# Performance work log

Hardware: AMD Instinct MI355X
Metric: run time of the kernel (lower is better)

The kernel has to match this reference:

```python
import jax, jax.numpy as jnp
import numpy as np

N, L = 131072, 4          # traffic lights, lanes per TL
E, H = 64, 128            # embed_dim, hidden_dim
NH, HD = 4, 16            # num_heads, head_dim (E = NH*HD)
NR, R = 4, 8              # num_regions, region_embed_dim
INIT_LOG_STD = -0.5


def _lin(k, fan_in, shape):
    b = 1.0 / np.sqrt(fan_in)
    return jax.random.uniform(k, shape, minval=-b, maxval=b, dtype=jnp.float32)


def setup_inputs() -> dict:
    key = jax.random.key(0)
    ks = jax.random.split(key, 32)
    inp = {
        "queue": jax.random.uniform(ks[0], (N, L), dtype=jnp.float32),
        "waiting": jax.random.uniform(ks[1], (N, L), dtype=jnp.float32),
        "phase_onehot": jax.random.uniform(ks[2], (N, 4), dtype=jnp.float32),
        "elapsed": jax.random.uniform(ks[3], (N,), dtype=jnp.float32),
        "region_ids": jax.random.randint(ks[4], (N,), 0, NR, dtype=jnp.int32),
        "noise": jax.random.normal(ks[5], (N,), dtype=jnp.float32),
        # lane_mlp: Linear(3,H) -> ReLU -> Linear(H,E) -> ReLU
        "lane_w1": _lin(ks[6], 3, (3, H)), "lane_b1": _lin(ks[7], 3, (H,)),
        "lane_w2": _lin(ks[8], H, (H, E)), "lane_b2": _lin(ks[9], H, (E,)),
        # MultiheadAttention in/out projections
        "attn_in_w": _lin(ks[10], E, (E, 3 * E)), "attn_in_b": jnp.zeros((3 * E,), jnp.float32),
        "attn_out_w": _lin(ks[11], E, (E, E)), "attn_out_b": jnp.zeros((E,), jnp.float32),
        # phase_mlp: Linear(5,H) -> ReLU -> Linear(H,H) -> ReLU
        "phase_w1": _lin(ks[12], 5, (5, H)), "phase_b1": _lin(ks[13], 5, (H,)),
        "phase_w2": _lin(ks[14], H, (H, H)), "phase_b2": _lin(ks[15], H, (H,)),
        # region embedding table
        "region_table": jax.random.normal(ks[16], (NR, R), dtype=jnp.float32),
        # mlp_head: Linear(E+H+R, H) -> ReLU -> Linear(H, 1)
        "head_w1": _lin(ks[17], E + H + R, (E + H + R, H)), "head_b1": _lin(ks[18], E + H + R, (H,)),
        "head_w2": _lin(ks[19], H, (H, 1)), "head_b2": _lin(ks[20], H, (1,)),
        "log_std": jnp.full((1,), INIT_LOG_STD, dtype=jnp.float32),
    }
    return inp


def reference(queue, waiting, phase_onehot, elapsed, region_ids, noise,
              lane_w1, lane_b1, lane_w2, lane_b2,
              attn_in_w, attn_in_b, attn_out_w, attn_out_b,
              phase_w1, phase_b1, phase_w2, phase_b2,
              region_table, head_w1, head_b1, head_w2, head_b2, log_std):
    # --- lane context: tiny MLP + self-attention over L lanes, batched over N TLs ---
    lane_feats = jnp.stack([queue, waiting, jnp.broadcast_to(elapsed[:, None], (N, L))], axis=-1)  # [N,L,3]
    h = jax.nn.relu(lane_feats @ lane_w1 + lane_b1)          # [N,L,H]
    emb = jax.nn.relu(h @ lane_w2 + lane_b2)                 # [N,L,E]

    qkv = emb @ attn_in_w + attn_in_b                        # [N,L,3E]
    q, k, v = jnp.split(qkv, 3, axis=-1)
    def heads(x):  # [N,L,E] -> [N,NH,L,HD]
        return x.reshape(N, L, NH, HD).transpose(0, 2, 1, 3)
    q, k, v = heads(q), heads(k), heads(v)
    scores = jnp.einsum('bhqd,bhkd->bhqk', q, k) / np.sqrt(HD)   # [N,NH,L,L]
    attn = jax.nn.softmax(scores, axis=-1)
    o = jnp.einsum('bhqk,bhkd->bhqd', attn, v)               # [N,NH,L,HD]
    o = o.transpose(0, 2, 1, 3).reshape(N, L, E)
    attn_out = o @ attn_out_w + attn_out_b                   # [N,L,E]
    ctx = attn_out.mean(axis=1)                              # [N,E]

    # --- phase MLP ---
    phase_elapsed = jnp.concatenate([phase_onehot, elapsed[:, None]], axis=-1)  # [N,5]
    ph = jax.nn.relu(phase_elapsed @ phase_w1 + phase_b1)
    phase_emb = jax.nn.relu(ph @ phase_w2 + phase_b2)        # [N,H]

    # --- region embedding (clamped index) ---
    rid = jnp.clip(region_ids, 0, NR - 1)
    region_emb = region_table[rid]                           # [N,R]

    # --- Gaussian head ---
    feat = jnp.concatenate([ctx, phase_emb, region_emb], axis=-1)  # [N,E+H+R]
    means = (jax.nn.relu(feat @ head_w1 + head_b1) @ head_w2 + head_b2)[:, 0]  # [N]

    ls = jnp.broadcast_to(log_std, means.shape)
    std = jnp.exp(ls)
    actions = means + std * noise
    actions_clamped = jnp.clip(actions, -1.0, 1.0)
    log_prob = -0.5 * ((actions - means) ** 2 / (std * std) + 2.0 * ls + np.log(2.0 * np.pi))
    return actions_clamped, log_prob
```

## Files before the change

### kernel.cpp

```cpp
#include <hip/hip_runtime.h>
#include <math.h>

#define N_TL 131072
#define GRID 2048
#define BLK 256

#define NFRAG 70
#define WS_CONST_OFF (NFRAG * 256)
#define NCONST 1346

typedef __attribute__((ext_vector_type(8))) short bfrag;
typedef __attribute__((ext_vector_type(4))) float f32x4;
typedef __attribute__((ext_vector_type(16))) float f32x16;

__device__ __forceinline__ unsigned short f2bf_rne(float x) {
  unsigned int u = __float_as_uint(x);
  return (unsigned short)((u + 0x7fffu + ((u >> 16) & 1u)) >> 16);
}
__device__ __forceinline__ unsigned int pack2(float a, float b) {
  return __builtin_amdgcn_perm(__float_as_uint(b) + 0x8000u,
                               __float_as_uint(a) + 0x8000u, 0x07060302u);
}
__device__ __forceinline__ float lo16(unsigned int u) { return __uint_as_float(u << 16); }
__device__ __forceinline__ float hi16(unsigned int u) { return __uint_as_float(u & 0xffff0000u); }
__device__ __forceinline__ f32x4 mfma16(bfrag a, bfrag b, f32x4 c) {
  return __builtin_amdgcn_mfma_f32_16x16x32_bf16(a, b, c, 0, 0, 0);
}
__device__ __forceinline__ f32x16 mfma32(bfrag a, bfrag b, f32x16 c) {
  return __builtin_amdgcn_mfma_f32_32x32x16_bf16(a, b, c, 0, 0, 0);
}

__device__ __forceinline__ bfrag load_wfragT(const float* __restrict__ w, int ncols,
                                             int col0, int k0, int lane, int K, float scale) {
  const int mm = lane & 15, qq = lane >> 4;
  bfrag f;
  #pragma unroll
  for (int j = 0; j < 8; ++j) {
    const int k = k0 + qq * 8 + j;
    const float v = (k < K) ? w[(size_t)k * ncols + col0 + mm] * scale : 0.f;
    f[j] = (short)f2bf_rne(v);
  }
  return f;
}
__device__ __forceinline__ bfrag load_wfragT32(const float* __restrict__ w, int ncols,
                                               int m0, int k0, int lane, int K, float scale) {
  const int mm = lane & 31, q1 = lane >> 5;
  bfrag f;
  #pragma unroll
  for (int j = 0; j < 8; ++j) {
    const int k = k0 + q1 * 8 + j;
    const float v = (k < K) ? w[(size_t)k * ncols + m0 + mm] * scale : 0.f;
    f[j] = (short)f2bf_rne(v);
  }
  return f;
}

__device__ __forceinline__ bfrag ldfrag(const uint4* __restrict__ WF, int f, int tid) {
  uint4 u = WF[f * 256 + tid];
  return *reinterpret_cast<bfrag*>(&u);
}

__device__ __forceinline__ bfrag ldb32f(const unsigned short* arr, int stride, int row,
                                        int kk, int q1) {
  return *reinterpret_cast<const bfrag*>(&arr[row * stride + kk * 16 + q1 * 8]);
}
__device__ __forceinline__ f32x16 binit32(const float* bias, int chBase, int q1) {
  f32x16 a;
  #pragma unroll
  for (int g = 0; g < 4; ++g) {
    const f32x4 bb = *reinterpret_cast<const f32x4*>(&bias[chBase + g * 8 + q1 * 4]);
    a[g * 4 + 0] = bb[0]; a[g * 4 + 1] = bb[1];
    a[g * 4 + 2] = bb[2]; a[g * 4 + 3] = bb[3];
  }
  return a;
}
__device__ __forceinline__ void st32(unsigned short* arr, int stride, int row,
                                     int chBase, int q1, f32x16 acc, bool relu) {
  #pragma unroll
  for (int g = 0; g < 4; ++g) {
    float a0 = acc[g * 4 + 0], a1 = acc[g * 4 + 1];
    float a2 = acc[g * 4 + 2], a3 = acc[g * 4 + 3];
    if (relu) {
      a0 = fmaxf(a0, 0.f); a1 = fmaxf(a1, 0.f);
      a2 = fmaxf(a2, 0.f); a3 = fmaxf(a3, 0.f);
    }
    uint2 u;
    u.x = pack2(a0, a1);
    u.y = pack2(a2, a3);
    *reinterpret_cast<uint2*>(&arr[row * stride + chBase + g * 8 + q1 * 4]) = u;
  }
}

#define LDBACT(arr, stride, nt, kk) \
  (*reinterpret_cast<const bfrag*>(&(arr)[((nt) * 16 + m) * (stride) + (kk) * 32 + quad * 8]))

__global__ __launch_bounds__(BLK)
void prep_weights(const float* __restrict__ lane_w1, const float* __restrict__ lane_b1,
                  const float* __restrict__ lane_w2, const float* __restrict__ lane_b2,
                  const float* __restrict__ attn_in_w, const float* __restrict__ attn_in_b,
                  const float* __restrict__ attn_out_w, const float* __restrict__ attn_out_b,
                  const float* __restrict__ phase_w1, const float* __restrict__ phase_b1,
                  const float* __restrict__ phase_w2, const float* __restrict__ phase_b2,
                  const float* __restrict__ region_table,
                  const float* __restrict__ head_w1, const float* __restrict__ head_b1,
                  const float* __restrict__ head_w2, const float* __restrict__ head_b2,
                  const float* __restrict__ log_std,
                  uint4* __restrict__ ws) {
  const int f = blockIdx.x;
  const int tid = threadIdx.x;
  const int wv = tid >> 6, lane = tid & 63;
  const int mb = wv >> 1;
  bfrag r;
  if (f < 8) {
    r = load_wfragT32(lane_w2, 64, mb * 32, f * 16, lane, 128, 1.f);
  } else if (f < 20) {
    const int t = (f - 8) >> 2, kk = (f - 8) & 3;
    r = load_wfragT32(attn_in_w, 192, (mb + 2 * t) * 32, kk * 16, lane, 64,
                      t == 0 ? 0.25f : 1.f);
  } else if (f < 22) {
    r = load_wfragT(attn_out_w, 64, wv * 16, (f - 20) * 32, lane, 64, 0.25f);
  } else if (f < 26) {
    const int t = (f - 22) >> 1, kk = (f - 22) & 1;
    r = load_wfragT32(lane_w1, 128, (mb + 2 * t) * 32, kk * 16, lane, 3, 1.f);
  } else if (f < 30) {
    const int t = (f - 26) >> 1, kk = (f - 26) & 1;
    r = load_wfragT32(phase_w1, 128, (mb + 2 * t) * 32, kk * 16, lane, 5, 1.f);
  } else if (f < 46) {
    const int t = (f - 30) >> 3, kk = (f - 30) & 7;
    r = load_wfragT32(phase_w2, 128, (mb + 2 * t) * 32, kk * 16, lane, 128, 1.f);
  } else {
    const int t = (f - 46) / 12, kk = (f - 46) % 12;
    r = load_wfragT32(head_w1, 128, (mb + 2 * t) * 32, kk * 16, lane, 192, 1.f);
  }
  ws[f * 256 + tid] = *reinterpret_cast<uint4*>(&r);

  if (f == 0) {
    float* wc = reinterpret_cast<float*>(ws + WS_CONST_OFF);
    for (int i = tid; i < NCONST; i += BLK) {
      float v;
      if (i < 128)       v = lane_b1[i];
      else if (i < 192)  v = lane_b2[i - 128];
      else if (i < 384)  { const int j = i - 192; v = attn_in_b[j] * ((j < 64) ? 0.25f : 1.f); }
      else if (i < 448)  v = attn_out_b[i - 384];
      else if (i < 576)  v = phase_b1[i - 448];
      else if (i < 704)  v = phase_b2[i - 576];
      else if (i < 1216) {
        const int g = (i - 704) >> 7, c = (i - 704) & 127;
        float a = head_b1[c];
        #pragma unroll
        for (int j = 0; j < 8; ++j) a += region_table[g * 8 + j] * head_w1[(192 + j) * 128 + c];
        v = a;
      }
      else if (i < 1344) v = head_w2[i - 1216];
      else if (i == 1344) v = head_b2[0];
      else               v = log_std[0];
      wc[i] = v;
    }
  }
}

struct alignas(16) SmemF {
  union {
    unsigned short qkv[64 * 200];
    unsigned short h[64 * 136];
    unsigned short ph[64 * 136];
  };
  unsigned short emb[64 * 72];
  unsigned short xbuf[64 * 40];
  unsigned short feat[64 * 200];
  float b1[128], b2[64], bin[192], bout[64];
  float pb1[128], pb2[128];
  float rbias[4][128];
  float hw2[128];
  float consts[2];
  int ridx[64];
};

__global__ __launch_bounds__(BLK, 2)
void fused_policy(const float* __restrict__ queue,
                  const float* __restrict__ waiting,
                  const float* __restrict__ phase_onehot,
                  const float* __restrict__ elapsed,
                  const int* __restrict__ region_ids,
                  const float* __restrict__ noise,
                  const uint4* __restrict__ WF,
                  float* __restrict__ out) {
  __shared__ SmemF S;
  const int tid  = threadIdx.x;
  const int wv   = tid >> 6;
  const int lane = tid & 63;
  const int m    = lane & 15;
  const int quad = lane >> 4;
  const int n32  = lane & 31;
  const int q1   = lane >> 5;
  const int mb   = wv >> 1;
  const int row64 = (wv & 1) * 32 + n32;
  const int n0   = blockIdx.x * 64;

  bfrag wL1[2][2], wL2[8], wQKV[3][4], wOUT2[2];
  #pragma unroll
  for (int kk = 0; kk < 8; ++kk) wL2[kk] = ldfrag(WF, kk, tid);
  #pragma unroll
  for (int t = 0; t < 3; ++t)
    #pragma unroll
    for (int kk = 0; kk < 4; ++kk) wQKV[t][kk] = ldfrag(WF, 8 + t * 4 + kk, tid);
  #pragma unroll
  for (int kk = 0; kk < 2; ++kk) wOUT2[kk] = ldfrag(WF, 20 + kk, tid);
  #pragma unroll
  for (int t = 0; t < 2; ++t)
    #pragma unroll
    for (int kk = 0; kk < 2; ++kk) wL1[t][kk] = ldfrag(WF, 22 + t * 2 + kk, tid);

  {
    const float2* src = reinterpret_cast<const float2*>(WF + WS_CONST_OFF);
    float2* dst = reinterpret_cast<float2*>(&S.b1[0]);
    for (int i = tid; i < NCONST / 2; i += BLK) dst[i] = src[i];
  }
  if (tid < 64) {
    int r = region_ids[n0 + tid];
    S.ridx[tid] = r < 0 ? 0 : (r > 3 ? 3 : r);
  }
  {
    const int r = tid >> 2, seg = tid & 3;
    uint4 z = {0, 0, 0, 0};
    if (seg == 0) {
      const int gl = n0 * 4 + r;
      z.x = pack2(queue[gl], waiting[gl]);
      z.y = pack2(elapsed[n0 + (r >> 2)], 0.f);
    }
    *reinterpret_cast<uint4*>(&S.xbuf[r * 40 + seg * 8]) = z;
  }
  __syncthreads();

  #pragma unroll 1
  for (int s = 0; s < 4; ++s) {
    const int tl0 = n0 + s * 16;

    {
      f32x16 acc[2];
      #pragma unroll
      for (int t = 0; t < 2; ++t) acc[t] = binit32(S.b1, (mb + 2 * t) * 32, q1);
      #pragma unroll
      for (int kk = 0; kk < 2; ++kk) {
        const bfrag b = ldb32f(S.xbuf, 40, row64, kk, q1);
        acc[0] = mfma32(wL1[0][kk], b, acc[0]);
        acc[1] = mfma32(wL1[1][kk], b, acc[1]);
      }
      #pragma unroll
      for (int t = 0; t < 2; ++t) st32(S.h, 136, row64, (mb + 2 * t) * 32, q1, acc[t], true);
    }
    __syncthreads();

    {
      f32x16 acc = binit32(S.b2, mb * 32, q1);
      #pragma unroll
      for (int kk = 0; kk < 8; ++kk)
        acc = mfma32(wL2[kk], ldb32f(S.h, 136, row64, kk, q1), acc);
      st32(S.emb, 72, row64, mb * 32, q1, acc, true);
    }
    __syncthreads();

    {
      f32x16 acc[3];
      #pragma unroll
      for (int t = 0; t < 3; ++t) acc[t] = binit32(S.bin, (mb + 2 * t) * 32, q1);
      #pragma unroll
      for (int kk = 0; kk < 4; ++kk) {
        const bfrag b = ldb32f(S.emb, 72, row64, kk, q1);
        #pragma unroll
        for (int t = 0; t < 3; ++t) acc[t] = mfma32(wQKV[t][kk], b, acc[t]);
      }
      #pragma unroll
      for (int t = 0; t < 3; ++t)
        st32(S.qkv, 200, row64, (mb + 2 * t) * 32, q1, acc[t], false);

      const int r = tid >> 2, seg = tid & 3;
      uint4 z = {0, 0, 0, 0};
      if (s < 3) {
        if (seg == 0) {
          const int gl = (tl0 + 16) * 4 + r;
          z.x = pack2(queue[gl], waiting[gl]);
          z.y = pack2(elapsed[tl0 + 16 + (r >> 2)], 0.f);
        }
      } else {
        if (seg == 0) {
          const float4 p = *reinterpret_cast<const float4*>(&phase_onehot[(n0 + r) * 4]);
          z.x = pack2(p.x, p.y);
          z.y = pack2(p.z, p.w);
          z.z = pack2(elapsed[n0 + r], 0.f);
        }
      }
      *reinterpret_cast<uint4*>(&S.xbuf[r * 40 + seg * 8]) = z;
    }
    __syncthreads();

    {
      const int tl = tid >> 4, l16 = tid & 15;
      const int hh = l16 >> 2, lq = l16 & 3;
      const uint4* qp = reinterpret_cast<const uint4*>(
          &S.qkv[(tl * 4 + lq) * 200 + hh * 16]);
      const uint4 qA = qp[0], qB = qp[1];
      const unsigned int qu[8] = {qA.x, qA.y, qA.z, qA.w, qB.x, qB.y, qB.z, qB.w};
      float qlo[8], qhi[8];
      #pragma unroll
      for (int j = 0; j < 8; ++j) { qlo[j] = lo16(qu[j]); qhi[j] = hi16(qu[j]); }
      float sc[4];
      #pragma unroll
      for (int lk = 0; lk < 4; ++lk) {
        const uint4* kp = reinterpret_cast<const uint4*>(
            &S.qkv[(tl * 4 + lk) * 200 + 64 + hh * 16]);
        const uint4 kA = kp[0], kB = kp[1];
        const unsigned int ku[8] = {kA.x, kA.y, kA.z, kA.w, kB.x, kB.y, kB.z, kB.w};
        float tx = 0.f, ty = 0.f;
        #pragma unroll
        for (int j = 0; j < 8; ++j) {
          tx += qlo[j] * lo16(ku[j]);
          ty += qhi[j] * hi16(ku[j]);
        }
        sc[lk] = tx + ty;
      }
      const float mx = fmaxf(fmaxf(sc[0], sc[1]), fmaxf(sc[2], sc[3]));
      const float e0 = __expf(sc[0] - mx), e1 = __expf(sc[1] - mx);
      const float e2 = __expf(sc[2] - mx), e3 = __expf(sc[3] - mx);
      const float inv = 1.f / (e0 + e1 + e2 + e3);
      const float pr[4] = {e0 * inv, e1 * inv, e2 * inv, e3 * inv};
      float olo[8], ohi[8];
      #pragma unroll
      for (int j = 0; j < 8; ++j) { olo[j] = 0.f; ohi[j] = 0.f; }
      #pragma unroll
      for (int lk = 0; lk < 4; ++lk) {
        const uint4* vp = reinterpret_cast<const uint4*>(
            &S.qkv[(tl * 4 + lk) * 200 + 128 + hh * 16]);
        const uint4 vA = vp[0], vB = vp[1];
        const unsigned int vu[8] = {vA.x, vA.y, vA.z, vA.w, vB.x, vB.y, vB.z, vB.w};
        const float p = pr[lk];
        #pragma unroll
        for (int j = 0; j < 8; ++j) {
          olo[j] += p * lo16(vu[j]);
          ohi[j] += p * hi16(vu[j]);
        }
      }
      unsigned short* om = S.emb;
      const int base = tl * 264 + lq * 64 + hh * 16;
      *reinterpret_cast<uint4*>(&om[base]) =
          make_uint4(pack2(olo[0], ohi[0]), pack2(olo[1], ohi[1]),
                     pack2(olo[2], ohi[2]), pack2(olo[3], ohi[3]));
      *reinterpret_cast<uint4*>(&om[base + 8]) =
          make_uint4(pack2(olo[4], ohi[4]), pack2(olo[5], ohi[5]),
                     pack2(olo[6], ohi[6]), pack2(olo[7], ohi[7]));
    }
    __syncthreads();

    {
      const int oc0 = wv * 16 + quad * 4;
      f32x4 acc = *reinterpret_cast<const f32x4*>(&S.bout[oc0]);
      #pragma unroll
      for (int kk = 0; kk < 8; ++kk)
        acc = mfma16(wOUT2[kk & 1], LDBACT(S.emb, 264, 0, kk), acc);
      uint2 u;
      u.x = pack2(acc[0], acc[1]);
      u.y = pack2(acc[2], acc[3]);
      *reinterpret_cast<uint2*>(&S.feat[(s * 16 + m) * 200 + oc0]) = u;
    }
  }
  __syncthreads();

  __builtin_amdgcn_sched_barrier(0);
  bfrag wP1[2][2], wP2[2][8], wH1[2][12];
  #pragma unroll
  for (int t = 0; t < 2; ++t) {
    #pragma unroll
    for (int kk = 0; kk < 2; ++kk)  wP1[t][kk] = ldfrag(WF, 26 + t * 2 + kk, tid);
    #pragma unroll
    for (int kk = 0; kk < 8; ++kk)  wP2[t][kk] = ldfrag(WF, 30 + t * 8 + kk, tid);
    #pragma unroll
    for (int kk = 0; kk < 12; ++kk) wH1[t][kk] = ldfrag(WF, 46 + t * 12 + kk, tid);
  }

  {
    f32x16 acc[2];
    #pragma unroll
    for (int t = 0; t < 2; ++t) acc[t] = binit32(S.pb1, (mb + 2 * t) * 32, q1);
    #pragma unroll
    for (int kk = 0; kk < 2; ++kk) {
      const bfrag b = ldb32f(S.xbuf, 40, row64, kk, q1);
      acc[0] = mfma32(wP1[0][kk], b, acc[0]);
      acc[1] = mfma32(wP1[1][kk], b, acc[1]);
    }
    #pragma unroll
    for (int t = 0; t < 2; ++t) st32(S.ph, 136, row64, (mb + 2 * t) * 32, q1, acc[t], true);
  }
  __syncthreads();

  {
    f32x16 acc[2];
    #pragma unroll
    for (int t = 0; t < 2; ++t) acc[t] = binit32(S.pb2, (mb + 2 * t) * 32, q1);
    #pragma unroll
    for (int kk = 0; kk < 8; ++kk) {
      const bfrag b = ldb32f(S.ph, 136, row64, kk, q1);
      acc[0] = mfma32(wP2[0][kk], b, acc[0]);
      acc[1] = mfma32(wP2[1][kk], b, acc[1]);
    }
    #pragma unroll
    for (int t = 0; t < 2; ++t)
      st32(S.feat, 200, row64, 64 + (mb + 2 * t) * 32, q1, acc[t], true);
  }
  __syncthreads();

  {
    const int g = S.ridx[row64];
    f32x16 acc[2];
    #pragma unroll
    for (int t = 0; t < 2; ++t) acc[t] = binit32(S.rbias[g], (mb + 2 * t) * 32, q1);
    #pragma unroll
    for (int kk = 0; kk < 12; ++kk) {
      const bfrag b = ldb32f(S.feat, 200, row64, kk, q1);
      acc[0] = mfma32(wH1[0][kk], b, acc[0]);
      acc[1] = mfma32(wH1[1][kk], b, acc[1]);
    }
    #pragma unroll
    for (int t = 0; t < 2; ++t) st32(S.ph, 136, row64, (mb + 2 * t) * 32, q1, acc[t], true);
  }
  __syncthreads();

  {
    const int tl = tid >> 2, s4 = tid & 3;
    const uint4* hp = reinterpret_cast<const uint4*>(&S.ph[tl * 136 + s4 * 32]);
    const uint4 h0 = hp[0], h1 = hp[1], h2 = hp[2], h3 = hp[3];
    const unsigned int hu[16] = {h0.x, h0.y, h0.z, h0.w, h1.x, h1.y, h1.z, h1.w,
                                 h2.x, h2.y, h2.z, h2.w, h3.x, h3.y, h3.z, h3.w};
    float t = 0.f;
    #pragma unroll
    for (int j = 0; j < 16; ++j) {
      t += lo16(hu[j]) * S.hw2[s4 * 32 + 2 * j];
      t += hi16(hu[j]) * S.hw2[s4 * 32 + 2 * j + 1];
    }
    t += __shfl_xor(t, 1);
    t += __shfl_xor(t, 2);
    if (s4 == 0) {
      const int n = n0 + tl;
      const float means = t + S.consts[0];
      const float ls = S.consts[1];
      const float nz = noise[n];
      const float a = means + __expf(ls) * nz;
      out[n] = fminf(fmaxf(a, -1.f), 1.f);
      out[N_TL + n] = -0.5f * (nz * nz + 2.f * ls + 1.8378770664093453f);
    }
  }
}

extern "C" void kernel_launch(void* const* d_in, const int* in_sizes, int n_in,
                              void* d_out, int out_size, void* d_ws, size_t ws_size,
                              hipStream_t stream) {
  const float* queue        = (const float*)d_in[0];
  const float* waiting      = (const float*)d_in[1];
  const float* phase_onehot = (const float*)d_in[2];
  const float* elapsed      = (const float*)d_in[3];
  const int*   region_ids   = (const int*)d_in[4];
  const float* noise        = (const float*)d_in[5];
  const float* lane_w1      = (const float*)d_in[6];
  const float* lane_b1      = (const float*)d_in[7];
  const float* lane_w2      = (const float*)d_in[8];
  const float* lane_b2      = (const float*)d_in[9];
  const float* attn_in_w    = (const float*)d_in[10];
  const float* attn_in_b    = (const float*)d_in[11];
  const float* attn_out_w   = (const float*)d_in[12];
  const float* attn_out_b   = (const float*)d_in[13];
  const float* phase_w1     = (const float*)d_in[14];
  const float* phase_b1     = (const float*)d_in[15];
  const float* phase_w2     = (const float*)d_in[16];
  const float* phase_b2     = (const float*)d_in[17];
  const float* region_table = (const float*)d_in[18];
  const float* head_w1      = (const float*)d_in[19];
  const float* head_b1      = (const float*)d_in[20];
  const float* head_w2      = (const float*)d_in[21];
  const float* head_b2      = (const float*)d_in[22];
  const float* log_std      = (const float*)d_in[23];

  float* out = (float*)d_out;
  uint4* ws  = (uint4*)d_ws;
  (void)ws_size;

  hipLaunchKernelGGL(prep_weights, dim3(NFRAG), dim3(BLK), 0, stream,
                     lane_w1, lane_b1, lane_w2, lane_b2,
                     attn_in_w, attn_in_b, attn_out_w, attn_out_b,
                     phase_w1, phase_b1, phase_w2, phase_b2, region_table,
                     head_w1, head_b1, head_w2, head_b2, log_std, ws);

  hipLaunchKernelGGL(fused_policy, dim3(GRID), dim3(BLK), 0, stream,
                     queue, waiting, phase_onehot, elapsed, region_ids, noise,
                     (const uint4*)ws, out);
}
```

Baseline: 191.0 us.

## Switch to per-wave 16x16 MFMA row ownership with wave-local syncs

Replaces the 32x32 MFMA tiling, where waves shared rows and needed block barriers, with a 16x16 MFMA layout in which each wave owns its own 16 rows through every stage. Most __syncthreads become wave-local waits on LDS counters, and inputs are loaded straight into register fragments instead of staging through an LDS buffer. Weight fragments are now streamed from global or L2 per stage instead of being held across the whole kernel, which lowers register pressure but adds repeated global loads. The 16x16 shape may give lower MFMA throughput per instruction than 32x32.

```diff
diff --git a/kernel.cpp b/kernel.cpp
--- a/kernel.cpp
+++ b/kernel.cpp
@@ -5,13 +5,17 @@
 #define GRID 2048
 #define BLK 256
 
-#define NFRAG 70
+#define NFRAG 138
 #define WS_CONST_OFF (NFRAG * 256)
 #define NCONST 1346
 
 typedef __attribute__((ext_vector_type(8))) short bfrag;
 typedef __attribute__((ext_vector_type(4))) float f32x4;
-typedef __attribute__((ext_vector_type(16))) float f32x16;
+
+#define WAVE_SYNC() do { \
+  asm volatile("s_waitcnt lgkmcnt(0)" ::: "memory"); \
+  __builtin_amdgcn_sched_barrier(0); \
+} while (0)
 
 __device__ __forceinline__ unsigned short f2bf_rne(float x) {
   unsigned int u = __float_as_uint(x);
@@ -25,9 +29,6 @@
 __device__ __forceinline__ float hi16(unsigned int u) { return __uint_as_float(u & 0xffff0000u); }
 __device__ __forceinline__ f32x4 mfma16(bfrag a, bfrag b, f32x4 c) {
   return __builtin_amdgcn_mfma_f32_16x16x32_bf16(a, b, c, 0, 0, 0);
-}
-__device__ __forceinline__ f32x16 mfma32(bfrag a, bfrag b, f32x16 c) {
-  return __builtin_amdgcn_mfma_f32_32x32x16_bf16(a, b, c, 0, 0, 0);
 }
 
 __device__ __forceinline__ bfrag load_wfragT(const float* __restrict__ w, int ncols,
@@ -42,57 +43,11 @@
   }
   return f;
 }
-__device__ __forceinline__ bfrag load_wfragT32(const float* __restrict__ w, int ncols,
-                                               int m0, int k0, int lane, int K, float scale) {
-  const int mm = lane & 31, q1 = lane >> 5;
-  bfrag f;
-  #pragma unroll
-  for (int j = 0; j < 8; ++j) {
-    const int k = k0 + q1 * 8 + j;
-    const float v = (k < K) ? w[(size_t)k * ncols + m0 + mm] * scale : 0.f;
-    f[j] = (short)f2bf_rne(v);
-  }
-  return f;
-}
 
 __device__ __forceinline__ bfrag ldfrag(const uint4* __restrict__ WF, int f, int tid) {
   uint4 u = WF[f * 256 + tid];
   return *reinterpret_cast<bfrag*>(&u);
 }
-
-__device__ __forceinline__ bfrag ldb32f(const unsigned short* arr, int stride, int row,
-                                        int kk, int q1) {
-  return *reinterpret_cast<const bfrag*>(&arr[row * stride + kk * 16 + q1 * 8]);
-}
-__device__ __forceinline__ f32x16 binit32(const float* bias, int chBase, int q1) {
-  f32x16 a;
-  #pragma unroll
-  for (int g = 0; g < 4; ++g) {
-    const f32x4 bb = *reinterpret_cast<const f32x4*>(&bias[chBase + g * 8 + q1 * 4]);
-    a[g * 4 + 0] = bb[0]; a[g * 4 + 1] = bb[1];
-    a[g * 4 + 2] = bb[2]; a[g * 4 + 3] = bb[3];
-  }
-  return a;
-}
-__device__ __forceinline__ void st32(unsigned short* arr, int stride, int row,
-                                     int chBase, int q1, f32x16 acc, bool relu) {
-  #pragma unroll
-  for (int g = 0; g < 4; ++g) {
-    float a0 = acc[g * 4 + 0], a1 = acc[g * 4 + 1];
-    float a2 = acc[g * 4 + 2], a3 = acc[g * 4 + 3];
-    if (relu) {
-      a0 = fmaxf(a0, 0.f); a1 = fmaxf(a1, 0.f);
-      a2 = fmaxf(a2, 0.f); a3 = fmaxf(a3, 0.f);
-    }
-    uint2 u;
-    u.x = pack2(a0, a1);
-    u.y = pack2(a2, a3);
-    *reinterpret_cast<uint2*>(&arr[row * stride + chBase + g * 8 + q1 * 4]) = u;
-  }
-}
-
-#define LDBACT(arr, stride, nt, kk) \
-  (*reinterpret_cast<const bfrag*>(&(arr)[((nt) * 16 + m) * (stride) + (kk) * 32 + quad * 8]))
 
 __global__ __launch_bounds__(BLK)
 void prep_weights(const float* __restrict__ lane_w1, const float* __restrict__ lane_b1,
@@ -109,28 +64,26 @@
   const int f = blockIdx.x;
   const int tid = threadIdx.x;
   const int wv = tid >> 6, lane = tid & 63;
-  const int mb = wv >> 1;
   bfrag r;
   if (f < 8) {
-    r = load_wfragT32(lane_w2, 64, mb * 32, f * 16, lane, 128, 1.f);
-  } else if (f < 20) {
-    const int t = (f - 8) >> 2, kk = (f - 8) & 3;
-    r = load_wfragT32(attn_in_w, 192, (mb + 2 * t) * 32, kk * 16, lane, 64,
-                      t == 0 ? 0.25f : 1.f);
-  } else if (f < 22) {
-    r = load_wfragT(attn_out_w, 64, wv * 16, (f - 20) * 32, lane, 64, 0.25f);
-  } else if (f < 26) {
-    const int t = (f - 22) >> 1, kk = (f - 22) & 1;
-    r = load_wfragT32(lane_w1, 128, (mb + 2 * t) * 32, kk * 16, lane, 3, 1.f);
-  } else if (f < 30) {
-    const int t = (f - 26) >> 1, kk = (f - 26) & 1;
-    r = load_wfragT32(phase_w1, 128, (mb + 2 * t) * 32, kk * 16, lane, 5, 1.f);
-  } else if (f < 46) {
-    const int t = (f - 30) >> 3, kk = (f - 30) & 7;
-    r = load_wfragT32(phase_w2, 128, (mb + 2 * t) * 32, kk * 16, lane, 128, 1.f);
+    r = load_wfragT(lane_w1, 128, f * 16, 0, lane, 3, 1.f);
+  } else if (f < 24) {
+    const int Mi = (f - 8) >> 2, kk = (f - 8) & 3;
+    r = load_wfragT(lane_w2, 64, Mi * 16, kk * 32, lane, 128, 1.f);
+  } else if (f < 48) {
+    const int Mi = (f - 24) >> 1, kk = (f - 24) & 1;
+    r = load_wfragT(attn_in_w, 192, Mi * 16, kk * 32, lane, 64,
+                    Mi < 4 ? 0.25f : 1.f);
+  } else if (f < 50) {
+    r = load_wfragT(attn_out_w, 64, wv * 16, (f - 48) * 32, lane, 64, 0.25f);
+  } else if (f < 58) {
+    r = load_wfragT(phase_w1, 128, (f - 50) * 16, 0, lane, 5, 1.f);
+  } else if (f < 90) {
+    const int Mi = (f - 58) >> 2, kk = (f - 58) & 3;
+    r = load_wfragT(phase_w2, 128, Mi * 16, kk * 32, lane, 128, 1.f);
   } else {
-    const int t = (f - 46) / 12, kk = (f - 46) % 12;
-    r = load_wfragT32(head_w1, 128, (mb + 2 * t) * 32, kk * 16, lane, 192, 1.f);
+    const int Mi = (f - 90) / 6, kk = (f - 90) % 6;
+    r = load_wfragT(head_w1, 128, Mi * 16, kk * 32, lane, 192, 1.f);
   }
   ws[f * 256 + tid] = *reinterpret_cast<uint4*>(&r);
 
@@ -166,14 +119,12 @@
     unsigned short ph[64 * 136];
   };
   unsigned short emb[64 * 72];
-  unsigned short xbuf[64 * 40];
   unsigned short feat[64 * 200];
   float b1[128], b2[64], bin[192], bout[64];
   float pb1[128], pb2[128];
   float rbias[4][128];
   float hw2[128];
   float consts[2];
-  int ridx[64];
 };
 
 __global__ __launch_bounds__(BLK, 2)
@@ -191,114 +142,102 @@
   const int lane = tid & 63;
   const int m    = lane & 15;
   const int quad = lane >> 4;
-  const int n32  = lane & 31;
-  const int q1   = lane >> 5;
-  const int mb   = wv >> 1;
-  const int row64 = (wv & 1) * 32 + n32;
   const int n0   = blockIdx.x * 64;
-
-  bfrag wL1[2][2], wL2[8], wQKV[3][4], wOUT2[2];
+  const int rloc = wv * 16 + m;
+
+  bfrag wL2[4][4];
   #pragma unroll
-  for (int kk = 0; kk < 8; ++kk) wL2[kk] = ldfrag(WF, kk, tid);
-  #pragma unroll
-  for (int t = 0; t < 3; ++t)
-    #pragma unroll
-    for (int kk = 0; kk < 4; ++kk) wQKV[t][kk] = ldfrag(WF, 8 + t * 4 + kk, tid);
-  #pragma unroll
-  for (int kk = 0; kk < 2; ++kk) wOUT2[kk] = ldfrag(WF, 20 + kk, tid);
-  #pragma unroll
-  for (int t = 0; t < 2; ++t)
-    #pragma unroll
-    for (int kk = 0; kk < 2; ++kk) wL1[t][kk] = ldfrag(WF, 22 + t * 2 + kk, tid);
+  for (int Mi = 0; Mi < 4; ++Mi)
+    #pragma unroll
+    for (int kk = 0; kk < 4; ++kk) wL2[Mi][kk] = ldfrag(WF, 8 + Mi * 4 + kk, tid);
 
   {
     const float2* src = reinterpret_cast<const float2*>(WF + WS_CONST_OFF);
     float2* dst = reinterpret_cast<float2*>(&S.b1[0]);
     for (int i = tid; i < NCONST / 2; i += BLK) dst[i] = src[i];
   }
-  if (tid < 64) {
-    int r = region_ids[n0 + tid];
-    S.ridx[tid] = r < 0 ? 0 : (r > 3 ? 3 : r);
-  }
-  {
-    const int r = tid >> 2, seg = tid & 3;
-    uint4 z = {0, 0, 0, 0};
-    if (seg == 0) {
-      const int gl = n0 * 4 + r;
-      z.x = pack2(queue[gl], waiting[gl]);
-      z.y = pack2(elapsed[n0 + (r >> 2)], 0.f);
-    }
-    *reinterpret_cast<uint4*>(&S.xbuf[r * 40 + seg * 8]) = z;
-  }
   __syncthreads();
 
   #pragma unroll 1
   for (int s = 0; s < 4; ++s) {
-    const int tl0 = n0 + s * 16;
-
     {
-      f32x16 acc[2];
-      #pragma unroll
-      for (int t = 0; t < 2; ++t) acc[t] = binit32(S.b1, (mb + 2 * t) * 32, q1);
-      #pragma unroll
-      for (int kk = 0; kk < 2; ++kk) {
-        const bfrag b = ldb32f(S.xbuf, 40, row64, kk, q1);
-        acc[0] = mfma32(wL1[0][kk], b, acc[0]);
-        acc[1] = mfma32(wL1[1][kk], b, acc[1]);
-      }
-      #pragma unroll
-      for (int t = 0; t < 2; ++t) st32(S.h, 136, row64, (mb + 2 * t) * 32, q1, acc[t], true);
-    }
-    __syncthreads();
+      bfrag wl1[8];
+      #pragma unroll
+      for (int Mi = 0; Mi < 8; ++Mi) wl1[Mi] = ldfrag(WF, Mi, tid);
+      uint4 z = {0, 0, 0, 0};
+      if (quad == 0) {
+        const int gl = (n0 + s * 16) * 4 + rloc;
+        z.x = pack2(queue[gl], waiting[gl]);
+        z.y = pack2(elapsed[n0 + s * 16 + (rloc >> 2)], 0.f);
+      }
+      const bfrag xf = *reinterpret_cast<bfrag*>(&z);
+      #pragma unroll
+      for (int Mi = 0; Mi < 8; ++Mi) {
+        f32x4 acc = *reinterpret_cast<const f32x4*>(&S.b1[Mi * 16 + quad * 4]);
+        acc = mfma16(wl1[Mi], xf, acc);
+        uint2 u;
+        u.x = pack2(fmaxf(acc[0], 0.f), fmaxf(acc[1], 0.f));
+        u.y = pack2(fmaxf(acc[2], 0.f), fmaxf(acc[3], 0.f));
+        *reinterpret_cast<uint2*>(&S.h[rloc * 136 + Mi * 16 + quad * 4]) = u;
+      }
+    }
+    WAVE_SYNC();
 
     {
-      f32x16 acc = binit32(S.b2, mb * 32, q1);
-      #pragma unroll
-      for (int kk = 0; kk < 8; ++kk)
-        acc = mfma32(wL2[kk], ldb32f(S.h, 136, row64, kk, q1), acc);
-      st32(S.emb, 72, row64, mb * 32, q1, acc, true);
-    }
-    __syncthreads();
+      f32x4 acc[4];
+      #pragma unroll
+      for (int Mi = 0; Mi < 4; ++Mi)
+        acc[Mi] = *reinterpret_cast<const f32x4*>(&S.b2[Mi * 16 + quad * 4]);
+      #pragma unroll
+      for (int kk = 0; kk < 4; ++kk) {
+        const bfrag b = *reinterpret_cast<const bfrag*>(
+            &S.h[rloc * 136 + kk * 32 + quad * 8]);
+        #pragma unroll
+        for (int Mi = 0; Mi < 4; ++Mi) acc[Mi] = mfma16(wL2[Mi][kk], b, acc[Mi]);
+      }
+      #pragma unroll
+      for (int Mi = 0; Mi < 4; ++Mi) {
+        uint2 u;
+        u.x = pack2(fmaxf(acc[Mi][0], 0.f), fmaxf(acc[Mi][1], 0.f));
+        u.y = pack2(fmaxf(acc[Mi][2], 0.f), fmaxf(acc[Mi][3], 0.f));
+        *reinterpret_cast<uint2*>(&S.emb[rloc * 72 + Mi * 16 + quad * 4]) = u;
+      }
+    }
+    WAVE_SYNC();
 
     {
-      f32x16 acc[3];
-      #pragma unroll
-      for (int t = 0; t < 3; ++t) acc[t] = binit32(S.bin, (mb + 2 * t) * 32, q1);
-      #pragma unroll
-      for (int kk = 0; kk < 4; ++kk) {
-        const bfrag b = ldb32f(S.emb, 72, row64, kk, q1);
-        #pragma unroll
-        for (int t = 0; t < 3; ++t) acc[t] = mfma32(wQKV[t][kk], b, acc[t]);
-      }
-      #pragma unroll
-      for (int t = 0; t < 3; ++t)
-        st32(S.qkv, 200, row64, (mb + 2 * t) * 32, q1, acc[t], false);
-
-      const int r = tid >> 2, seg = tid & 3;
-      uint4 z = {0, 0, 0, 0};
-      if (s < 3) {
-        if (seg == 0) {
-          const int gl = (tl0 + 16) * 4 + r;
-          z.x = pack2(queue[gl], waiting[gl]);
-          z.y = pack2(elapsed[tl0 + 16 + (r >> 2)], 0.f);
+      const bfrag e0 = *reinterpret_cast<const bfrag*>(&S.emb[rloc * 72 + quad * 8]);
+      const bfrag e1 = *reinterpret_cast<const bfrag*>(&S.emb[rloc * 72 + 32 + quad * 8]);
+      #pragma unroll
+      for (int half = 0; half < 2; ++half) {
+        bfrag wq[6][2];
+        #pragma unroll
+        for (int i = 0; i < 6; ++i)
+          #pragma unroll
+          for (int kk = 0; kk < 2; ++kk)
+            wq[i][kk] = ldfrag(WF, 24 + (half * 6 + i) * 2 + kk, tid);
+        #pragma unroll
+        for (int i = 0; i < 6; ++i) {
+          const int Mi = half * 6 + i;
+          f32x4 acc = *reinterpret_cast<const f32x4*>(&S.bin[Mi * 16 + quad * 4]);
+          acc = mfma16(wq[i][0], e0, acc);
+          acc = mfma16(wq[i][1], e1, acc);
+          uint2 u;
+          u.x = pack2(acc[0], acc[1]);
+          u.y = pack2(acc[2], acc[3]);
+          *reinterpret_cast<uint2*>(&S.qkv[rloc * 200 + Mi * 16 + quad * 4]) = u;
         }
-      } else {
-        if (seg == 0) {
-          const float4 p = *reinterpret_cast<const float4*>(&phase_onehot[(n0 + r) * 4]);
-          z.x = pack2(p.x, p.y);
-          z.y = pack2(p.z, p.w);
-          z.z = pack2(elapsed[n0 + r], 0.f);
-        }
-      }
-      *reinterpret_cast<uint4*>(&S.xbuf[r * 40 + seg * 8]) = z;
-    }
-    __syncthreads();
+      }
+    }
+    WAVE_SYNC();
 
     {
-      const int tl = tid >> 4, l16 = tid & 15;
-      const int hh = l16 >> 2, lq = l16 & 3;
+      const int tlq = lane >> 4;
+      const int hh  = (lane >> 2) & 3;
+      const int lq  = lane & 3;
+      const int rb  = wv * 16 + tlq * 4;
       const uint4* qp = reinterpret_cast<const uint4*>(
-          &S.qkv[(tl * 4 + lq) * 200 + hh * 16]);
+          &S.qkv[(rb + lq) * 200 + hh * 16]);
       const uint4 qA = qp[0], qB = qp[1];
       const unsigned int qu[8] = {qA.x, qA.y, qA.z, qA.w, qB.x, qB.y, qB.z, qB.w};
       float qlo[8], qhi[8];
@@ -308,7 +247,7 @@
       #pragma unroll
       for (int lk = 0; lk < 4; ++lk) {
         const uint4* kp = reinterpret_cast<const uint4*>(
-            &S.qkv[(tl * 4 + lk) * 200 + 64 + hh * 16]);
+            &S.qkv[(rb + lk) * 200 + 64 + hh * 16]);
         const uint4 kA = kp[0], kB = kp[1];
         const unsigned int ku[8] = {kA.x, kA.y, kA.z, kA.w, kB.x, kB.y, kB.z, kB.w};
         float tx = 0.f, ty = 0.f;
@@ -330,7 +269,7 @@
       #pragma unroll
       for (int lk = 0; lk < 4; ++lk) {
         const uint4* vp = reinterpret_cast<const uint4*>(
-            &S.qkv[(tl * 4 + lk) * 200 + 128 + hh * 16]);
+            &S.qkv[(rb + lk) * 200 + 128 + hh * 16]);
         const uint4 vA = vp[0], vB = vp[1];
         const unsigned int vu[8] = {vA.x, vA.y, vA.z, vA.w, vB.x, vB.y, vB.z, vB.w};
         const float p = pr[lk];
@@ -340,8 +279,8 @@
           ohi[j] += p * hi16(vu[j]);
         }
       }
-      unsigned short* om = S.emb;
-      const int base = tl * 264 + lq * 64 + hh * 16;
+      unsigned short* om = S.emb + wv * 1152;
+      const int base = tlq * 264 + lq * 64 + hh * 16;
       *reinterpret_cast<uint4*>(&om[base]) =
           make_uint4(pack2(olo[0], ohi[0]), pack2(olo[1], ohi[1]),
                      pack2(olo[2], ohi[2]), pack2(olo[3], ohi[3]));
@@ -352,81 +291,105 @@
     __syncthreads();
 
     {
+      bfrag wo[2];
+      #pragma unroll
+      for (int kk = 0; kk < 2; ++kk) wo[kk] = ldfrag(WF, 48 + kk, tid);
       const int oc0 = wv * 16 + quad * 4;
       f32x4 acc = *reinterpret_cast<const f32x4*>(&S.bout[oc0]);
-      #pragma unroll
-      for (int kk = 0; kk < 8; ++kk)
-        acc = mfma16(wOUT2[kk & 1], LDBACT(S.emb, 264, 0, kk), acc);
+      const unsigned short* omr = S.emb + (m >> 2) * 1152 + (m & 3) * 264;
+      #pragma unroll
+      for (int kk = 0; kk < 8; ++kk) {
+        const bfrag b = *reinterpret_cast<const bfrag*>(&omr[kk * 32 + quad * 8]);
+        acc = mfma16(wo[kk & 1], b, acc);
+      }
       uint2 u;
       u.x = pack2(acc[0], acc[1]);
       u.y = pack2(acc[2], acc[3]);
       *reinterpret_cast<uint2*>(&S.feat[(s * 16 + m) * 200 + oc0]) = u;
     }
-  }
-  __syncthreads();
-
-  __builtin_amdgcn_sched_barrier(0);
-  bfrag wP1[2][2], wP2[2][8], wH1[2][12];
-  #pragma unroll
-  for (int t = 0; t < 2; ++t) {
-    #pragma unroll
-    for (int kk = 0; kk < 2; ++kk)  wP1[t][kk] = ldfrag(WF, 26 + t * 2 + kk, tid);
-    #pragma unroll
-    for (int kk = 0; kk < 8; ++kk)  wP2[t][kk] = ldfrag(WF, 30 + t * 8 + kk, tid);
-    #pragma unroll
-    for (int kk = 0; kk < 12; ++kk) wH1[t][kk] = ldfrag(WF, 46 + t * 12 + kk, tid);
+    __syncthreads();
   }
 
   {
-    f32x16 acc[2];
-    #pragma unroll
-    for (int t = 0; t < 2; ++t) acc[t] = binit32(S.pb1, (mb + 2 * t) * 32, q1);
-    #pragma unroll
-    for (int kk = 0; kk < 2; ++kk) {
-      const bfrag b = ldb32f(S.xbuf, 40, row64, kk, q1);
-      acc[0] = mfma32(wP1[0][kk], b, acc[0]);
-      acc[1] = mfma32(wP1[1][kk], b, acc[1]);
-    }
-    #pragma unroll
-    for (int t = 0; t < 2; ++t) st32(S.ph, 136, row64, (mb + 2 * t) * 32, q1, acc[t], true);
-  }
-  __syncthreads();
+    bfrag wp1[8];
+    #pragma unroll
+    for (int Mi = 0; Mi < 8; ++Mi) wp1[Mi] = ldfrag(WF, 50 + Mi, tid);
+    uint4 z = {0, 0, 0, 0};
+    if (quad == 0) {
+      const float4 p = *reinterpret_cast<const float4*>(&phase_onehot[(n0 + rloc) * 4]);
+      z.x = pack2(p.x, p.y);
+      z.y = pack2(p.z, p.w);
+      z.z = pack2(elapsed[n0 + rloc], 0.f);
+    }
+    const bfrag pf = *reinterpret_cast<bfrag*>(&z);
+    #pragma unroll
+    for (int Mi = 0; Mi < 8; ++Mi) {
+      f32x4 acc = *reinterpret_cast<const f32x4*>(&S.pb1[Mi * 16 + quad * 4]);
+      acc = mfma16(wp1[Mi], pf, acc);
+      uint2 u;
+      u.x = pack2(fmaxf(acc[0], 0.f), fmaxf(acc[1], 0.f));
+      u.y = pack2(fmaxf(acc[2], 0.f), fmaxf(acc[3], 0.f));
+      *reinterpret_cast<uint2*>(&S.ph[rloc * 136 + Mi * 16 + quad * 4]) = u;
+    }
+  }
+  WAVE_SYNC();
 
   {
-    f32x16 acc[2];
-    #pragma unroll
-    for (int t = 0; t < 2; ++t) acc[t] = binit32(S.pb2, (mb + 2 * t) * 32, q1);
-    #pragma unroll
-    for (int kk = 0; kk < 8; ++kk) {
-      const bfrag b = ldb32f(S.ph, 136, row64, kk, q1);
-      acc[0] = mfma32(wP2[0][kk], b, acc[0]);
-      acc[1] = mfma32(wP2[1][kk], b, acc[1]);
-    }
-    #pragma unroll
-    for (int t = 0; t < 2; ++t)
-      st32(S.feat, 200, row64, 64 + (mb + 2 * t) * 32, q1, acc[t], true);
-  }
-  __syncthreads();
+    f32x4 acc[8];
+    #pragma unroll
+    for (int Mi = 0; Mi < 8; ++Mi)
+      acc[Mi] = *reinterpret_cast<const f32x4*>(&S.pb2[Mi * 16 + quad * 4]);
+    #pragma unroll
+    for (int kk = 0; kk < 4; ++kk) {
+      bfrag wk[8];
+      #pragma unroll
+      for (int Mi = 0; Mi < 8; ++Mi) wk[Mi] = ldfrag(WF, 58 + Mi * 4 + kk, tid);
+      const bfrag b = *reinterpret_cast<const bfrag*>(
+          &S.ph[rloc * 136 + kk * 32 + quad * 8]);
+      #pragma unroll
+      for (int Mi = 0; Mi < 8; ++Mi) acc[Mi] = mfma16(wk[Mi], b, acc[Mi]);
+    }
+    #pragma unroll
+    for (int Mi = 0; Mi < 8; ++Mi) {
+      uint2 u;
+      u.x = pack2(fmaxf(acc[Mi][0], 0.f), fmaxf(acc[Mi][1], 0.f));
+      u.y = pack2(fmaxf(acc[Mi][2], 0.f), fmaxf(acc[Mi][3], 0.f));
+      *reinterpret_cast<uint2*>(&S.feat[rloc * 200 + 64 + Mi * 16 + quad * 4]) = u;
+    }
+  }
+  WAVE_SYNC();
 
   {
-    const int g = S.ridx[row64];
-    f32x16 acc[2];
-    #pragma unroll
-    for (int t = 0; t < 2; ++t) acc[t] = binit32(S.rbias[g], (mb + 2 * t) * 32, q1);
-    #pragma unroll
-    for (int kk = 0; kk < 12; ++kk) {
-      const bfrag b = ldb32f(S.feat, 200, row64, kk, q1);
-      acc[0] = mfma32(wH1[0][kk], b, acc[0]);
-      acc[1] = mfma32(wH1[1][kk], b, acc[1]);
-    }
-    #pragma unroll
-    for (int t = 0; t < 2; ++t) st32(S.ph, 136, row64, (mb + 2 * t) * 32, q1, acc[t], true);
-  }
-  __syncthreads();
+    int rg = region_ids[n0 + rloc];
+    rg = rg < 0 ? 0 : (rg > 3 ? 3 : rg);
+    f32x4 acc[8];
+    #pragma unroll
+    for (int Mi = 0; Mi < 8; ++Mi)
+      acc[Mi] = *reinterpret_cast<const f32x4*>(&S.rbias[rg][Mi * 16 + quad * 4]);
+    #pragma unroll
+    for (int kk = 0; kk < 6; ++kk) {
+      bfrag wk[8];
+      #pragma unroll
+      for (int Mi = 0; Mi < 8; ++Mi) wk[Mi] = ldfrag(WF, 90 + Mi * 6 + kk, tid);
+      const bfrag b = *reinterpret_cast<const bfrag*>(
+          &S.feat[rloc * 200 + kk * 32 + quad * 8]);
+      #pragma unroll
+      for (int Mi = 0; Mi < 8; ++Mi) acc[Mi] = mfma16(wk[Mi], b, acc[Mi]);
+    }
+    #pragma unroll
+    for (int Mi = 0; Mi < 8; ++Mi) {
+      uint2 u;
+      u.x = pack2(fmaxf(acc[Mi][0], 0.f), fmaxf(acc[Mi][1], 0.f));
+      u.y = pack2(fmaxf(acc[Mi][2], 0.f), fmaxf(acc[Mi][3], 0.f));
+      *reinterpret_cast<uint2*>(&S.ph[rloc * 136 + Mi * 16 + quad * 4]) = u;
+    }
+  }
+  WAVE_SYNC();
 
   {
-    const int tl = tid >> 2, s4 = tid & 3;
-    const uint4* hp = reinterpret_cast<const uint4*>(&S.ph[tl * 136 + s4 * 32]);
+    const int tl = lane >> 2, s4 = lane & 3;
+    const int row = wv * 16 + tl;
+    const uint4* hp = reinterpret_cast<const uint4*>(&S.ph[row * 136 + s4 * 32]);
     const uint4 h0 = hp[0], h1 = hp[1], h2 = hp[2], h3 = hp[3];
     const unsigned int hu[16] = {h0.x, h0.y, h0.z, h0.w, h1.x, h1.y, h1.z, h1.w,
                                  h2.x, h2.y, h2.z, h2.w, h3.x, h3.y, h3.z, h3.w};
@@ -439,7 +402,7 @@
     t += __shfl_xor(t, 1);
     t += __shfl_xor(t, 2);
     if (s4 == 0) {
-      const int n = n0 + tl;
+      const int n = n0 + row;
       const float means = t + S.consts[0];
       const float ls = S.consts[1];
       const float nz = noise[n];
```

Result: slower. 209.2 us (+9.5%).

## Shrink shared memory footprint to allow three blocks per CU

Applied to the files above, without the earlier changes.

Removes the large 64x200 feat buffer by keeping attention context in a smaller ctx buffer and writing the phase MLP output into the dead tail of the qkv union. The head layer now reads its K range from two sources. The xbuf stride, hw2 staging and ridx staging are dropped, with hw2 and region ids read from global memory instead. Launch bounds go from 2 to 3 blocks per CU to raise occupancy, which tightens the per-thread register budget and may cause spills given the many weight fragments held in registers.

```diff
diff --git a/kernel.cpp b/kernel.cpp
--- a/kernel.cpp
+++ b/kernel.cpp
@@ -166,17 +166,15 @@
     unsigned short ph[64 * 136];
   };
   unsigned short emb[64 * 72];
-  unsigned short xbuf[64 * 40];
-  unsigned short feat[64 * 200];
+  unsigned short xbuf[64 * 32];
+  unsigned short ctx[64 * 72];
   float b1[128], b2[64], bin[192], bout[64];
   float pb1[128], pb2[128];
   float rbias[4][128];
-  float hw2[128];
   float consts[2];
-  int ridx[64];
 };
 
-__global__ __launch_bounds__(BLK, 2)
+__global__ __launch_bounds__(BLK, 3)
 void fused_policy(const float* __restrict__ queue,
                   const float* __restrict__ waiting,
                   const float* __restrict__ phase_onehot,
@@ -196,6 +194,9 @@
   const int mb   = wv >> 1;
   const int row64 = (wv & 1) * 32 + n32;
   const int n0   = blockIdx.x * 64;
+  const float* wsf = reinterpret_cast<const float*>(WF + WS_CONST_OFF);
+  unsigned short* pl2out =
+      reinterpret_cast<unsigned short*>(reinterpret_cast<char*>(&S) + 64 * 136 * 2);
 
   bfrag wL1[2][2], wL2[8], wQKV[3][4], wOUT2[2];
   #pragma unroll
@@ -212,14 +213,11 @@
     for (int kk = 0; kk < 2; ++kk) wL1[t][kk] = ldfrag(WF, 22 + t * 2 + kk, tid);
 
   {
-    const float2* src = reinterpret_cast<const float2*>(WF + WS_CONST_OFF);
+    const float2* src = reinterpret_cast<const float2*>(wsf);
     float2* dst = reinterpret_cast<float2*>(&S.b1[0]);
-    for (int i = tid; i < NCONST / 2; i += BLK) dst[i] = src[i];
-  }
-  if (tid < 64) {
-    int r = region_ids[n0 + tid];
-    S.ridx[tid] = r < 0 ? 0 : (r > 3 ? 3 : r);
-  }
+    for (int i = tid; i < 608; i += BLK) dst[i] = src[i];
+  }
+  if (tid < 2) S.consts[tid] = wsf[1344 + tid];
   {
     const int r = tid >> 2, seg = tid & 3;
     uint4 z = {0, 0, 0, 0};
@@ -228,7 +226,7 @@
       z.x = pack2(queue[gl], waiting[gl]);
       z.y = pack2(elapsed[n0 + (r >> 2)], 0.f);
     }
-    *reinterpret_cast<uint4*>(&S.xbuf[r * 40 + seg * 8]) = z;
+    *reinterpret_cast<uint4*>(&S.xbuf[r * 32 + seg * 8]) = z;
   }
   __syncthreads();
 
@@ -242,7 +240,7 @@
       for (int t = 0; t < 2; ++t) acc[t] = binit32(S.b1, (mb + 2 * t) * 32, q1);
       #pragma unroll
       for (int kk = 0; kk < 2; ++kk) {
-        const bfrag b = ldb32f(S.xbuf, 40, row64, kk, q1);
+        const bfrag b = ldb32f(S.xbuf, 32, row64, kk, q1);
         acc[0] = mfma32(wL1[0][kk], b, acc[0]);
         acc[1] = mfma32(wL1[1][kk], b, acc[1]);
       }
@@ -290,7 +288,7 @@
           z.z = pack2(elapsed[n0 + r], 0.f);
         }
       }
-      *reinterpret_cast<uint4*>(&S.xbuf[r * 40 + seg * 8]) = z;
+      *reinterpret_cast<uint4*>(&S.xbuf[r * 32 + seg * 8]) = z;
     }
     __syncthreads();
 
@@ -360,7 +358,7 @@
       uint2 u;
       u.x = pack2(acc[0], acc[1]);
       u.y = pack2(acc[2], acc[3]);
-      *reinterpret_cast<uint2*>(&S.feat[(s * 16 + m) * 200 + oc0]) = u;
+      *reinterpret_cast<uint2*>(&S.ctx[(s * 16 + m) * 72 + oc0]) = u;
     }
   }
   __syncthreads();
@@ -383,7 +381,7 @@
     for (int t = 0; t < 2; ++t) acc[t] = binit32(S.pb1, (mb + 2 * t) * 32, q1);
     #pragma unroll
     for (int kk = 0; kk < 2; ++kk) {
-      const bfrag b = ldb32f(S.xbuf, 40, row64, kk, q1);
+      const bfrag b = ldb32f(S.xbuf, 32, row64, kk, q1);
       acc[0] = mfma32(wP1[0][kk], b, acc[0]);
       acc[1] = mfma32(wP1[1][kk], b, acc[1]);
     }
@@ -404,28 +402,36 @@
     }
     #pragma unroll
     for (int t = 0; t < 2; ++t)
-      st32(S.feat, 200, row64, 64 + (mb + 2 * t) * 32, q1, acc[t], true);
+      st32(pl2out, 136, row64, (mb + 2 * t) * 32, q1, acc[t], true);
   }
   __syncthreads();
 
   {
-    const int g = S.ridx[row64];
+    int rg = region_ids[n0 + row64];
+    rg = rg < 0 ? 0 : (rg > 3 ? 3 : rg);
     f32x16 acc[2];
     #pragma unroll
-    for (int t = 0; t < 2; ++t) acc[t] = binit32(S.rbias[g], (mb + 2 * t) * 32, q1);
-    #pragma unroll
-    for (int kk = 0; kk < 12; ++kk) {
-      const bfrag b = ldb32f(S.feat, 200, row64, kk, q1);
+    for (int t = 0; t < 2; ++t) acc[t] = binit32(S.rbias[rg], (mb + 2 * t) * 32, q1);
+    #pragma unroll
+    for (int kk = 0; kk < 4; ++kk) {
+      const bfrag b = ldb32f(S.ctx, 72, row64, kk, q1);
       acc[0] = mfma32(wH1[0][kk], b, acc[0]);
       acc[1] = mfma32(wH1[1][kk], b, acc[1]);
     }
     #pragma unroll
+    for (int kk = 4; kk < 12; ++kk) {
+      const bfrag b = ldb32f(pl2out, 136, row64, kk - 4, q1);
+      acc[0] = mfma32(wH1[0][kk], b, acc[0]);
+      acc[1] = mfma32(wH1[1][kk], b, acc[1]);
+    }
+    #pragma unroll
     for (int t = 0; t < 2; ++t) st32(S.ph, 136, row64, (mb + 2 * t) * 32, q1, acc[t], true);
   }
   __syncthreads();
 
   {
     const int tl = tid >> 2, s4 = tid & 3;
+    const float* hw2g = wsf + 1216;
     const uint4* hp = reinterpret_cast<const uint4*>(&S.ph[tl * 136 + s4 * 32]);
     const uint4 h0 = hp[0], h1 = hp[1], h2 = hp[2], h3 = hp[3];
     const unsigned int hu[16] = {h0.x, h0.y, h0.z, h0.w, h1.x, h1.y, h1.z, h1.w,
@@ -433,8 +439,8 @@
     float t = 0.f;
     #pragma unroll
     for (int j = 0; j < 16; ++j) {
-      t += lo16(hu[j]) * S.hw2[s4 * 32 + 2 * j];
-      t += hi16(hu[j]) * S.hw2[s4 * 32 + 2 * j + 1];
+      t += lo16(hu[j]) * hw2g[s4 * 32 + 2 * j];
+      t += hi16(hu[j]) * hw2g[s4 * 32 + 2 * j + 1];
     }
     t += __shfl_xor(t, 1);
     t += __shfl_xor(t, 2);
```

After: 215.8 us. +13.0%, slower.
